# Performance work log

Hardware: AMD Instinct MI355X
Metric: run time of the kernel (lower is better)

## Reference

```python
import jax, jax.numpy as jnp
import numpy as np

FIELD_DIMS = [4000] * 24
EMBED_DIM = 32
BATCH = 4096
VOCAB = sum(FIELD_DIMS)
NUM_FIELDS = len(FIELD_DIMS)


def setup_inputs() -> dict:
    key = jax.random.key(0)
    k_x, k_ffm, k_fc = jax.random.split(key, 3)
    x = jax.random.randint(k_x, (BATCH, NUM_FIELDS), 0, 4000, dtype=jnp.int64)
    offsets = jnp.asarray(np.concatenate([[0], np.cumsum(FIELD_DIMS)[:-1]]), dtype=jnp.int64)
    # xavier_normal for [VOCAB, EMBED_DIM] tables: std = sqrt(2/(fan_in+fan_out))
    std = float(np.sqrt(2.0 / (VOCAB + EMBED_DIM)))
    ffm_W = jax.random.normal(k_ffm, (NUM_FIELDS, VOCAB, EMBED_DIM), dtype=jnp.float32) * std
    fc_W = jax.random.normal(k_fc, (VOCAB, 1), dtype=jnp.float32) * 0.01
    bias = jnp.zeros((1,), dtype=jnp.float32)
    return {"x": x, "offsets": offsets, "ffm_W": ffm_W, "fc_W": fc_W, "bias": bias}


def reference(x, offsets, ffm_W, fc_W, bias):
    idx = x + offsets[None, :]                      # [B, F] global ids
    # gather every table at every field id: [F_table, B, F_field, D] -> [B, Ft, Ff, D]
    P = jnp.transpose(jnp.take(ffm_W, idx, axis=1), (1, 0, 2, 3))
    # pair (i,j): emb_table_j[field_i] * emb_table_i[field_j], summed over D
    S = jnp.einsum('bijd,bjid->bij', P, P)          # [B, F, F], symmetric
    F = S.shape[1]
    upper = jnp.triu(jnp.ones((F, F), dtype=bool), k=1)
    ffm_term = jnp.sum(jnp.where(upper, S, 0.0), axis=(1, 2))[:, None]  # [B, 1]
    lin = jnp.sum(jnp.take(fc_W, idx, axis=0), axis=1) + bias           # [B, 1]
    return jax.nn.sigmoid(jnp.squeeze(lin + ffm_term, axis=1))          # [B]
```

## Files before the change

### kernel.cpp

```cpp
#include <hip/hip_runtime.h>
#include <math.h>

#define NBATCH  4096
#define NFIELDS 24
#define EMBED   32
#define NVOCAB  96000
#define NPAIRS  ((NFIELDS * (NFIELDS - 1)) / 2)

__global__ __launch_bounds__(256) void ffm_fwd_kernel(
    const int* __restrict__ x,
    const int* __restrict__ offsets,
    const float* __restrict__ ffm_W,
    const float* __restrict__ fc_W,
    const float* __restrict__ bias,
    float* __restrict__ out)
{
    const int b   = blockIdx.x;
    const int tid = threadIdx.x;

    __shared__ int           s_ids[NFIELDS];
    __shared__ unsigned char s_pi[NPAIRS];
    __shared__ unsigned char s_pj[NPAIRS];
    __shared__ float         s_wsum[4];

    for (int p = tid; p < NPAIRS; p += 256) {
        int i = 0, rem = p;
        while (rem >= NFIELDS - 1 - i) { rem -= NFIELDS - 1 - i; ++i; }
        s_pi[p] = (unsigned char)i;
        s_pj[p] = (unsigned char)(i + 1 + rem);
    }

    float local = 0.0f;
    if (tid < NFIELDS) {
        const int id = x[b * NFIELDS + tid] + offsets[tid];
        s_ids[tid] = id;
        local = fc_W[id];
    }
    __syncthreads();

    const int group = tid >> 3;
    const int lane8 = tid & 7;

    #pragma unroll
    for (int it = 0; it < 8; ++it) {
        const int p = group + it * 32;
        const int i = s_pi[p];
        const int j = s_pj[p];
        const float4 av = *(const float4*)(ffm_W +
            ((long long)i * NVOCAB + s_ids[j]) * EMBED + lane8 * 4);
        const float4 bv = *(const float4*)(ffm_W +
            ((long long)j * NVOCAB + s_ids[i]) * EMBED + lane8 * 4);
        local += av.x * bv.x + av.y * bv.y + av.z * bv.z + av.w * bv.w;
    }
    {
        const int p = group + 256;
        if (p < NPAIRS) {
            const int i = s_pi[p];
            const int j = s_pj[p];
            const float4 av = *(const float4*)(ffm_W +
                ((long long)i * NVOCAB + s_ids[j]) * EMBED + lane8 * 4);
            const float4 bv = *(const float4*)(ffm_W +
                ((long long)j * NVOCAB + s_ids[i]) * EMBED + lane8 * 4);
            local += av.x * bv.x + av.y * bv.y + av.z * bv.z + av.w * bv.w;
        }
    }

    #pragma unroll
    for (int off = 32; off > 0; off >>= 1)
        local += __shfl_xor(local, off);
    if ((tid & 63) == 0) s_wsum[tid >> 6] = local;
    __syncthreads();
    if (tid == 0) {
        const float z = s_wsum[0] + s_wsum[1] + s_wsum[2] + s_wsum[3] + bias[0];
        out[b] = 1.0f / (1.0f + __expf(-z));
    }
}

extern "C" void kernel_launch(void* const* d_in, const int* in_sizes, int n_in,
                              void* d_out, int out_size, void* d_ws, size_t ws_size,
                              hipStream_t stream) {
    const int*   x       = (const int*)d_in[0];
    const int*   offsets = (const int*)d_in[1];
    const float* ffm_W   = (const float*)d_in[2];
    const float* fc_W    = (const float*)d_in[3];
    const float* bias    = (const float*)d_in[4];
    float*       out     = (float*)d_out;

    ffm_fwd_kernel<<<NBATCH, 256, 0, stream>>>(x, offsets, ffm_W, fc_W, bias, out);
}
```

Baseline: 52.67 us.

## Split FFM into pair-major gather kernel plus finalize reduction kernel

```diff
diff --git a/kernel.cpp b/kernel.cpp
--- a/kernel.cpp
+++ b/kernel.cpp
@@ -7,73 +7,93 @@
 #define NVOCAB  96000
 #define NPAIRS  ((NFIELDS * (NFIELDS - 1)) / 2)
 
-__global__ __launch_bounds__(256) void ffm_fwd_kernel(
+#define CHUNKS        64
+#define SAMP_PER_BLK  (NBATCH / CHUNKS)
+#define PAIRS_MAIN    34
+
+__global__ __launch_bounds__(256) void ffm_pairs_kernel(
     const int* __restrict__ x,
     const int* __restrict__ offsets,
     const float* __restrict__ ffm_W,
-    const float* __restrict__ fc_W,
-    const float* __restrict__ bias,
-    float* __restrict__ out)
+    float* __restrict__ part)
 {
-    const int b   = blockIdx.x;
     const int tid = threadIdx.x;
+    const int x8  = blockIdx.x & 7;
+    const int o   = blockIdx.x >> 3;
 
-    __shared__ int           s_ids[NFIELDS];
-    __shared__ unsigned char s_pi[NPAIRS];
-    __shared__ unsigned char s_pj[NPAIRS];
-    __shared__ float         s_wsum[4];
-
-    for (int p = tid; p < NPAIRS; p += 256) {
-        int i = 0, rem = p;
-        while (rem >= NFIELDS - 1 - i) { rem -= NFIELDS - 1 - i; ++i; }
-        s_pi[p] = (unsigned char)i;
-        s_pj[p] = (unsigned char)(i + 1 + rem);
+    int pair, chunk;
+    const int pl = o / CHUNKS;
+    if (pl < PAIRS_MAIN) {
+        pair  = pl * 8 + x8;
+        chunk = o - pl * CHUNKS;
+    } else {
+        const int r = (o - PAIRS_MAIN * CHUNKS) + x8 * (CHUNKS / 2);
+        pair  = 272 + (r >> 6);
+        chunk = r & (CHUNKS - 1);
     }
 
-    float local = 0.0f;
-    if (tid < NFIELDS) {
-        const int id = x[b * NFIELDS + tid] + offsets[tid];
-        s_ids[tid] = id;
-        local = fc_W[id];
+    int i = 0, rem = pair;
+    while (rem >= NFIELDS - 1 - i) { rem -= NFIELDS - 1 - i; ++i; }
+    const int j = i + 1 + rem;
+
+    const int b0 = chunk * SAMP_PER_BLK;
+
+    __shared__ int s_aid[SAMP_PER_BLK];
+    __shared__ int s_bid[SAMP_PER_BLK];
+
+    if (tid < SAMP_PER_BLK) {
+        s_bid[tid] = x[(b0 + tid) * NFIELDS + i] + offsets[i];
+    } else if (tid < 2 * SAMP_PER_BLK) {
+        const int t = tid - SAMP_PER_BLK;
+        s_aid[t] = x[(b0 + t) * NFIELDS + j] + offsets[j];
     }
     __syncthreads();
 
-    const int group = tid >> 3;
-    const int lane8 = tid & 7;
+    const int g  = tid >> 3;
+    const int l4 = (tid & 7) * 4;
 
     #pragma unroll
-    for (int it = 0; it < 8; ++it) {
-        const int p = group + it * 32;
-        const int i = s_pi[p];
-        const int j = s_pj[p];
+    for (int k = 0; k < SAMP_PER_BLK / 32; ++k) {
+        const int bl = k * 32 + g;
         const float4 av = *(const float4*)(ffm_W +
-            ((long long)i * NVOCAB + s_ids[j]) * EMBED + lane8 * 4);
+            ((long long)i * NVOCAB + s_aid[bl]) * EMBED + l4);
         const float4 bv = *(const float4*)(ffm_W +
-            ((long long)j * NVOCAB + s_ids[i]) * EMBED + lane8 * 4);
-        local += av.x * bv.x + av.y * bv.y + av.z * bv.z + av.w * bv.w;
+            ((long long)j * NVOCAB + s_bid[bl]) * EMBED + l4);
+        float d = av.x * bv.x + av.y * bv.y + av.z * bv.z + av.w * bv.w;
+        d += __shfl_xor(d, 1);
+        d += __shfl_xor(d, 2);
+        d += __shfl_xor(d, 4);
+        if ((tid & 7) == 0)
+            part[(long long)pair * NBATCH + b0 + bl] = d;
     }
-    {
-        const int p = group + 256;
-        if (p < NPAIRS) {
-            const int i = s_pi[p];
-            const int j = s_pj[p];
-            const float4 av = *(const float4*)(ffm_W +
-                ((long long)i * NVOCAB + s_ids[j]) * EMBED + lane8 * 4);
-            const float4 bv = *(const float4*)(ffm_W +
-                ((long long)j * NVOCAB + s_ids[i]) * EMBED + lane8 * 4);
-            local += av.x * bv.x + av.y * bv.y + av.z * bv.z + av.w * bv.w;
-        }
+}
+
+__global__ __launch_bounds__(256) void ffm_finalize_kernel(
+    const int* __restrict__ x,
+    const int* __restrict__ offsets,
+    const float* __restrict__ fc_W,
+    const float* __restrict__ bias,
+    const float* __restrict__ part,
+    float* __restrict__ out)
+{
+    const int b = blockIdx.x * 256 + threadIdx.x;
+
+    float lin = bias[0];
+    #pragma unroll
+    for (int f = 0; f < NFIELDS; ++f)
+        lin += fc_W[x[b * NFIELDS + f] + offsets[f]];
+
+    const float* pb = part + b;
+    float s0 = 0.f, s1 = 0.f, s2 = 0.f, s3 = 0.f;
+    #pragma unroll 4
+    for (int p = 0; p < NPAIRS; p += 4) {
+        s0 += pb[(long long)(p + 0) * NBATCH];
+        s1 += pb[(long long)(p + 1) * NBATCH];
+        s2 += pb[(long long)(p + 2) * NBATCH];
+        s3 += pb[(long long)(p + 3) * NBATCH];
     }
-
-    #pragma unroll
-    for (int off = 32; off > 0; off >>= 1)
-        local += __shfl_xor(local, off);
-    if ((tid & 63) == 0) s_wsum[tid >> 6] = local;
-    __syncthreads();
-    if (tid == 0) {
-        const float z = s_wsum[0] + s_wsum[1] + s_wsum[2] + s_wsum[3] + bias[0];
-        out[b] = 1.0f / (1.0f + __expf(-z));
-    }
+    const float z = lin + ((s0 + s1) + (s2 + s3));
+    out[b] = 1.0f / (1.0f + __expf(-z));
 }
 
 extern "C" void kernel_launch(void* const* d_in, const int* in_sizes, int n_in,
@@ -85,6 +105,8 @@
     const float* fc_W    = (const float*)d_in[3];
     const float* bias    = (const float*)d_in[4];
     float*       out     = (float*)d_out;
+    float*       part    = (float*)d_ws;
 
-    ffm_fwd_kernel<<<NBATCH, 256, 0, stream>>>(x, offsets, ffm_W, fc_W, bias, out);
+    ffm_pairs_kernel<<<NPAIRS * CHUNKS, 256, 0, stream>>>(x, offsets, ffm_W, part);
+    ffm_finalize_kernel<<<NBATCH / 256, 256, 0, stream>>>(x, offsets, fc_W, bias, part, out);
 }
```

New measurement: 52.12 us. Within noise of the previous version (-1.1%).
